# Kernel tuning notes

Measured on AMD Instinct MI355X. Metric: run time of the kernel, lower is better.

Reference implementation:

```python
import jax, jax.numpy as jnp
import numpy as np

N0, N1, N2 = 120000, 24000, 6000  # nodes per sampled layer
H1, C1 = 8, 64   # layer1: heads, nhid (concat -> 512)
H2, C2 = 8, 256  # layer2: out heads, code_embed_dim (mean over heads)
D = 256
NEG_SLOPE = 0.2


def gat_conv(x_src, x_dst, src, dst, W, att_src, att_dst, bias, n_tgt, concat):
    H, C = att_src.shape
    h_src = (x_src @ W).reshape(-1, H, C)   # [N_src, H, C]
    h_dst = (x_dst @ W).reshape(-1, H, C)   # [N_tgt, H, C]
    a_src = jnp.einsum('nhc,hc->nh', h_src, att_src)  # [N_src, H]
    a_dst = jnp.einsum('nhc,hc->nh', h_dst, att_dst)  # [N_tgt, H]
    e = a_src[src] + a_dst[dst]                       # [E, H]
    e = jnp.where(e > 0, e, NEG_SLOPE * e)            # LeakyReLU
    # segment softmax over edges grouped by target node
    m = jax.ops.segment_max(e, dst, num_segments=n_tgt)  # [N_tgt, H]
    ex = jnp.exp(e - m[dst])
    denom = jax.ops.segment_sum(ex, dst, num_segments=n_tgt)
    alpha = ex / denom[dst]                           # [E, H]
    msg = alpha[:, :, None] * h_src[src]              # [E, H, C]
    out = jax.ops.segment_sum(msg, dst, num_segments=n_tgt)  # [N_tgt, H, C]
    if concat:
        return out.reshape(n_tgt, H * C) + bias
    return out.mean(axis=1) + bias


def setup_inputs() -> dict:
    key = jax.random.key(0)
    ks = jax.random.split(key, 12)
    E1, E2 = 384000, 96000
    g1 = 1.0 / np.sqrt(D)
    g2 = 1.0 / np.sqrt(H1 * C1)
    return {
        'x': jax.random.normal(ks[0], (N0, D), jnp.float32),
        'src1': jax.random.randint(ks[1], (E1,), 0, N0),
        'dst1': jax.random.randint(ks[2], (E1,), 0, N1),
        'src2': jax.random.randint(ks[3], (E2,), 0, N1),
        'dst2': jax.random.randint(ks[4], (E2,), 0, N2),
        'W1': jax.random.normal(ks[5], (D, H1 * C1), jnp.float32) * g1,
        'att_src1': jax.random.normal(ks[6], (H1, C1), jnp.float32) * 0.1,
        'att_dst1': jax.random.normal(ks[7], (H1, C1), jnp.float32) * 0.1,
        'b1': jnp.zeros((H1 * C1,), jnp.float32),
        'W2': jax.random.normal(ks[8], (H1 * C1, H2 * C2), jnp.float32) * g2,
        'att_src2': jax.random.normal(ks[9], (H2, C2), jnp.float32) * 0.1,
        'att_dst2': jax.random.normal(ks[10], (H2, C2), jnp.float32) * 0.1,
        'b2': jnp.zeros((C2,), jnp.float32),
    }


def reference(x, src1, dst1, src2, dst2, W1, att_src1, att_dst1, b1,
              W2, att_src2, att_dst2, b2):
    # layer 1: bipartite conv (x, x[:N1]), concat heads, then ELU
    x1 = gat_conv(x, x[:N1], src1, dst1, W1, att_src1, att_dst1, b1, N1, True)
    x1 = jax.nn.elu(x1)
    # layer 2: (x1, x1[:N2]), mean over heads
    x2 = gat_conv(x1, x1[:N2], src2, dst2, W2, att_src2, att_dst2, b2, N2, False)
    return x2
```

## Files before the change

### kernel.cpp

```cpp
#include <hip/hip_runtime.h>
#include <hip/hip_bf16.h>
#include <cstdint>

typedef __attribute__((ext_vector_type(8))) short short8;
typedef __attribute__((ext_vector_type(4))) float floatx4;
typedef __hip_bfloat16 bf16;
typedef unsigned short u16;

static constexpr int cN0 = 120000, cN1 = 24000, cN2 = 6000;
static constexpr int cD = 256, cHC1 = 512;
static constexpr int CH1 = 4800;

__device__ __forceinline__ float dot4(float4 a, float4 b) {
  return a.x * b.x + a.y * b.y + a.z * b.z + a.w * b.w;
}

__global__ __launch_bounds__(256)
void gat_prep(const float* __restrict__ W1, const float* __restrict__ W2,
              const float* __restrict__ as1, const float* __restrict__ ad1,
              const float* __restrict__ as2, const float* __restrict__ ad2,
              u16* __restrict__ W1t, u16* __restrict__ W2te,
              float* __restrict__ wts1, float* __restrict__ wtd1,
              float* __restrict__ wts2, float* __restrict__ wtd2) {
  __shared__ u16 tile[32][33];
  int b = (int)blockIdx.x;
  if (b < 512) {
    int t = b * 256 + threadIdx.x;
    int n = t >> 8, k = t & 255;
    bf16 v = bf16(W1[(size_t)k * 512 + n]);
    W1t[t] = *(u16*)&v;
    return;
  }
  b -= 512;
  if (b < 1024) {
    int bx = b & 15, by = (b >> 4) & 7, h = b >> 7;
    int kt = bx * 32, ct = by * 32;
    int tx = threadIdx.x & 31, ty4 = (threadIdx.x >> 5) * 4;
#pragma unroll
    for (int i = 0; i < 4; i++) {
      int k = kt + ty4 + i, c = ct + tx;
      bf16 v = bf16(W2[(size_t)k * 2048 + h * 256 + c]);
      tile[ty4 + i][tx] = *(u16*)&v;
    }
    __syncthreads();
#pragma unroll
    for (int i = 0; i < 4; i++) {
      int c = ct + ty4 + i, k = kt + tx;
      W2te[(size_t)c * 4096 + h * 512 + k] = tile[tx][ty4 + i];
    }
    return;
  }
  b -= 1024;
  int lane = threadIdx.x & 63;
  int K, Ch, ldw, task;
  const float *W, *as, *ad;
  float *ws, *wd;
  if (b < 512) {
    K = 256; Ch = 64; ldw = 512; W = W1; as = as1; ad = ad1; ws = wts1; wd = wtd1;
    task = b * 4 + (threadIdx.x >> 6);
  } else {
    b -= 512;
    K = 512; Ch = 256; ldw = 2048; W = W2; as = as2; ad = ad2; ws = wts2; wd = wtd2;
    task = b * 4 + (threadIdx.x >> 6);
  }
  if (task >= 8 * K) return;
  int h = task / K, k = task - h * K;
  const float* Wr = W + (size_t)k * ldw + h * Ch;
  const float* asp = as + h * Ch;
  const float* adp = ad + h * Ch;
  float ss = 0.f, dd = 0.f;
  for (int c = lane; c < Ch; c += 64) {
    float wv = Wr[c];
    ss += wv * asp[c];
    dd += wv * adp[c];
  }
#pragma unroll
  for (int o = 32; o; o >>= 1) { ss += __shfl_down(ss, o); dd += __shfl_down(dd, o); }
  if (lane == 0) { ws[task] = ss; wd[task] = dd; }
}

#define RSTAGE(HALF, MASK)                                              \
  {                                                                     \
    _Pragma("unroll") for (int j = 0; j < HALF; j++) {                  \
      float send = (lane & MASK) ? v[j] : v[j + HALF];                  \
      float rcv = __shfl_xor(send, MASK);                               \
      v[j] = ((lane & MASK) ? v[j + HALF] : v[j]) + rcv;                \
    }                                                                   \
  }

__global__ __launch_bounds__(256)
void gat_scores_reg(const float* __restrict__ x, const float* __restrict__ wsrc,
                    const float* __restrict__ wdst, float* __restrict__ a_s,
                    float* __restrict__ a_d, int M, int MD) {
  int lane = threadIdx.x & 63;
  int wv = (blockIdx.x * 256 + threadIdx.x) >> 6;
  int nw = (gridDim.x * 256) >> 6;
  float4 w[16];
#pragma unroll
  for (int j = 0; j < 8; j++) {
    w[j]     = *(const float4*)&wsrc[j * 256 + lane * 4];
    w[j + 8] = *(const float4*)&wdst[j * 256 + lane * 4];
  }
  for (int row = wv; row < M; row += nw) {
    float4 xv = *(const float4*)&x[(size_t)row * 256 + lane * 4];
    float v[16];
#pragma unroll
    for (int j = 0; j < 16; j++) v[j] = dot4(xv, w[j]);
    RSTAGE(8, 1) RSTAGE(4, 2) RSTAGE(2, 4) RSTAGE(1, 8)
    v[0] += __shfl_xor(v[0], 16);
    v[0] += __shfl_xor(v[0], 32);
    if (lane < 16) {
      int o = ((lane & 1) << 3) | ((lane & 2) << 1) | ((lane & 4) >> 1) | ((lane & 8) >> 3);
      if (o < 8) a_s[row * 8 + o] = v[0];
      else if (row < MD) a_d[row * 8 + (o - 8)] = v[0];
    }
  }
}

__global__ __launch_bounds__(256)
void gat_scores_w512(const float* __restrict__ x, const float* __restrict__ wsrc,
                     const float* __restrict__ wdst, float* __restrict__ a_s,
                     float* __restrict__ a_d, int M, int MD) {
  __shared__ float wl[16 * 512];
  int tid = threadIdx.x;
#pragma unroll
  for (int base = 0; base < 8192; base += 1024) {
    int idx = base + tid * 4;
    int j = idx >> 9, c = idx & 511;
    *(float4*)&wl[idx] = (j < 8) ? *(const float4*)&wsrc[j * 512 + c]
                                 : *(const float4*)&wdst[(j - 8) * 512 + c];
  }
  __syncthreads();
  int lane = tid & 63;
  int wv = (blockIdx.x * 256 + tid) >> 6;
  int nw = (gridDim.x * 256) >> 6;
  for (int row = wv; row < M; row += nw) {
    float4 xa = *(const float4*)&x[(size_t)row * 512 + lane * 4];
    float4 xb = *(const float4*)&x[(size_t)row * 512 + 256 + lane * 4];
    float v[16];
#pragma unroll
    for (int j = 0; j < 16; j++) {
      float4 wa = *(const float4*)&wl[j * 512 + lane * 4];
      float4 wb = *(const float4*)&wl[j * 512 + 256 + lane * 4];
      v[j] = dot4(xa, wa) + dot4(xb, wb);
    }
    RSTAGE(8, 1) RSTAGE(4, 2) RSTAGE(2, 4) RSTAGE(1, 8)
    v[0] += __shfl_xor(v[0], 16);
    v[0] += __shfl_xor(v[0], 32);
    if (lane < 16) {
      int o = ((lane & 1) << 3) | ((lane & 2) << 1) | ((lane & 4) >> 1) | ((lane & 8) >> 3);
      if (o < 8) a_s[row * 8 + o] = v[0];
      else if (row < MD) a_d[row * 8 + (o - 8)] = v[0];
    }
  }
}

__global__ __launch_bounds__(256)
void gat_hist(const int* __restrict__ dstv, int* __restrict__ cnt, int E) {
  int t = blockIdx.x * 256 + threadIdx.x;
  if (t < E) atomicAdd(&cnt[dstv[t]], 1);
}

__global__ __launch_bounds__(1024)
void gat_scan1(const int* __restrict__ cnt, int* __restrict__ off,
               int* __restrict__ bsum, int n) {
  __shared__ int wsum[16];
  int t = threadIdx.x, lane = t & 63, wid = t >> 6;
  int idx = blockIdx.x * 1024 + t;
  int v = (idx < n) ? cnt[idx] : 0;
  int x = v;
#pragma unroll
  for (int d = 1; d < 64; d <<= 1) { int y = __shfl_up(x, d); if (lane >= d) x += y; }
  if (lane == 63) wsum[wid] = x;
  __syncthreads();
  if (t < 16) {
    int s = wsum[t];
#pragma unroll
    for (int d = 1; d < 16; d <<= 1) { int y = __shfl_up(s, d); if (t >= d) s += y; }
    wsum[t] = s;
  }
  __syncthreads();
  int excl = (wid ? wsum[wid - 1] : 0) + x - v;
  if (idx < n) off[idx] = excl;
  if (t == 1023) bsum[blockIdx.x] = wsum[15];
}

__global__ __launch_bounds__(256)
void gat_scan3(int* __restrict__ off, const int* __restrict__ bsum, int n, int nb) {
  int i = blockIdx.x * 256 + threadIdx.x;
  int blk = (blockIdx.x * 256) >> 10;
  int add = 0;
  for (int b = 0; b < blk; b++) add += bsum[b];
  if (i < n) off[i] += add;
  if (i == 0) {
    int tot = 0;
    for (int b = 0; b < nb; b++) tot += bsum[b];
    off[n] = tot;
  }
}

__global__ __launch_bounds__(256)
void gat_scatter_edge(const int* __restrict__ src, const int* __restrict__ dstv,
                      const float* __restrict__ a_s, const float* __restrict__ a_d,
                      const int* __restrict__ off, int* __restrict__ cur,
                      int* __restrict__ srcs, float* __restrict__ exs, int E) {
  int t = blockIdx.x * 256 + threadIdx.x;
  if (t >= E) return;
  int s = src[t], d = dstv[t];
  int slot = off[d] + atomicAdd(&cur[d], 1);
  srcs[slot] = s;
  const float* as = a_s + (size_t)s * 8;
  const float* ad = a_d + (size_t)d * 8;
  float4 s0 = *(const float4*)as, s1 = *(const float4*)(as + 4);
  float4 d0 = *(const float4*)ad, d1 = *(const float4*)(ad + 4);
  float ev[8] = { s0.x + d0.x, s0.y + d0.y, s0.z + d0.z, s0.w + d0.w,
                  s1.x + d1.x, s1.y + d1.y, s1.z + d1.z, s1.w + d1.w };
  float exv[8];
#pragma unroll
  for (int h = 0; h < 8; h++) {
    float e = ev[h];
    e = e > 0.f ? e : 0.2f * e;
    exv[h] = expf(e);
  }
  float4* op = (float4*)(exs + (size_t)slot * 8);
  op[0] = make_float4(exv[0], exv[1], exv[2], exv[3]);
  op[1] = make_float4(exv[4], exv[5], exv[6], exv[7]);
}

__global__ __launch_bounds__(256)
void gat_denom(const float* __restrict__ exs, const int* __restrict__ off,
               float* __restrict__ den, int N) {
  int lane = threadIdx.x & 63;
  int d = blockIdx.x * 4 + (threadIdx.x >> 6);
  if (d >= N) return;
  int beg = off[d], end = off[d + 1];
  float s = 0.f;
  for (size_t idx = (size_t)beg * 8 + lane; idx < (size_t)end * 8; idx += 64)
    s += exs[idx];
#pragma unroll
  for (int o = 32; o >= 8; o >>= 1) s += __shfl_down(s, o);
  if (lane < 8) den[(size_t)d * 8 + lane] = s;
}

template<int CDIM>
__global__ __launch_bounds__(CDIM)
void gat_gather(const float* __restrict__ x, const float* __restrict__ exs,
                const float* __restrict__ den, const int* __restrict__ off,
                const int* __restrict__ srcs, u16* __restrict__ agg, int d0) {
  int d = d0 + blockIdx.x, t = threadIdx.x;
  int beg = off[d], end = off[d + 1];
  float inv[8];
#pragma unroll
  for (int j = 0; j < 8; j++) {
    float dv = den[(size_t)d * 8 + j];
    inv[j] = dv > 0.f ? 1.f / dv : 0.f;
  }
  float acc[8] = {};
  const float* xb = x + t;
  int i = beg;
  for (; i + 4 <= end; i += 4) {
    int s0 = srcs[i], s1 = srcs[i + 1], s2 = srcs[i + 2], s3 = srcs[i + 3];
    float xv0 = xb[(size_t)s0 * CDIM];
    float xv1 = xb[(size_t)s1 * CDIM];
    float xv2 = xb[(size_t)s2 * CDIM];
    float xv3 = xb[(size_t)s3 * CDIM];
    float4 e0a = *(const float4*)&exs[(size_t)i * 8];
    float4 e0b = *(const float4*)&exs[(size_t)i * 8 + 4];
    float4 e1a = *(const float4*)&exs[(size_t)(i + 1) * 8];
    float4 e1b = *(const float4*)&exs[(size_t)(i + 1) * 8 + 4];
    float4 e2a = *(const float4*)&exs[(size_t)(i + 2) * 8];
    float4 e2b = *(const float4*)&exs[(size_t)(i + 2) * 8 + 4];
    float4 e3a = *(const float4*)&exs[(size_t)(i + 3) * 8];
    float4 e3b = *(const float4*)&exs[(size_t)(i + 3) * 8 + 4];
    acc[0] += e0a.x * xv0 + e1a.x * xv1 + e2a.x * xv2 + e3a.x * xv3;
    acc[1] += e0a.y * xv0 + e1a.y * xv1 + e2a.y * xv2 + e3a.y * xv3;
    acc[2] += e0a.z * xv0 + e1a.z * xv1 + e2a.z * xv2 + e3a.z * xv3;
    acc[3] += e0a.w * xv0 + e1a.w * xv1 + e2a.w * xv2 + e3a.w * xv3;
    acc[4] += e0b.x * xv0 + e1b.x * xv1 + e2b.x * xv2 + e3b.x * xv3;
    acc[5] += e0b.y * xv0 + e1b.y * xv1 + e2b.y * xv2 + e3b.y * xv3;
    acc[6] += e0b.z * xv0 + e1b.z * xv1 + e2b.z * xv2 + e3b.z * xv3;
    acc[7] += e0b.w * xv0 + e1b.w * xv1 + e2b.w * xv2 + e3b.w * xv3;
  }
  for (; i < end; i++) {
    int s = srcs[i];
    float xv = xb[(size_t)s * CDIM];
    float4 ea = *(const float4*)&exs[(size_t)i * 8];
    float4 eb = *(const float4*)&exs[(size_t)i * 8 + 4];
    acc[0] += ea.x * xv; acc[1] += ea.y * xv; acc[2] += ea.z * xv; acc[3] += ea.w * xv;
    acc[4] += eb.x * xv; acc[5] += eb.y * xv; acc[6] += eb.z * xv; acc[7] += eb.w * xv;
  }
  u16* ap = agg + (size_t)blockIdx.x * (8 * CDIM) + t;
#pragma unroll
  for (int j = 0; j < 8; j++) {
    bf16 v = bf16(acc[j] * inv[j]);
    ap[(size_t)j * CDIM] = *(u16*)&v;
  }
}

template<int BN, int EPI>
__global__ __launch_bounds__(256)
void gat_gemm(const u16* __restrict__ A, long lda, const u16* __restrict__ Bt, long ldb,
              float* __restrict__ C, long ldc, int M, int K,
              const float* __restrict__ bias, int zA, int zB, long zC, int zBias) {
  __shared__ __align__(16) u16 Al[64 * 64];
  __shared__ __align__(16) u16 Bl[BN * 64];
  const int tid = threadIdx.x;
  const int bm = blockIdx.x << 6;
  const int n0 = blockIdx.y * BN;
  const int z = blockIdx.z;
  const u16* Ab = A + (size_t)z * zA;
  const u16* Bb = Bt + (size_t)z * zB + (size_t)n0 * ldb;
  const int wid = tid >> 6, lane = tid & 63;
  const int wm = (wid & 1) << 5, wn = (wid >> 1) * (BN / 2);
  const int q = lane >> 4, r = lane & 15;
  constexpr int NJ = BN / 32;
  floatx4 acc[2][NJ] = {};
  const int arow = tid >> 3;
  const int chunk = tid & 7;
  const int acol = chunk << 3;
  for (int k0 = 0; k0 < K; k0 += 64) {
    __syncthreads();
#pragma unroll
    for (int rr = 0; rr < 2; rr++) {
      int row = arow + rr * 32;
      int gr = bm + row; if (gr >= M) gr = M - 1;
      *(uint4*)&Al[row * 64 + ((chunk ^ (row & 7)) << 3)] =
          *(const uint4*)&Ab[(size_t)gr * lda + k0 + acol];
    }
#pragma unroll
    for (int rr = 0; rr < BN / 32; rr++) {
      int row = arow + rr * 32;
      *(uint4*)&Bl[row * 64 + ((chunk ^ (row & 7)) << 3)] =
          *(const uint4*)&Bb[(size_t)row * ldb + k0 + acol];
    }
    __syncthreads();
#pragma unroll
    for (int kk = 0; kk < 64; kk += 32) {
      const int cs = (((kk >> 3) + q) ^ (r & 7)) << 3;
      short8 af[2], bfr[NJ];
#pragma unroll
      for (int i = 0; i < 2; i++)  af[i]  = *(const short8*)&Al[(wm + i * 16 + r) * 64 + cs];
#pragma unroll
      for (int j = 0; j < NJ; j++) bfr[j] = *(const short8*)&Bl[(wn + j * 16 + r) * 64 + cs];
#pragma unroll
      for (int i = 0; i < 2; i++)
#pragma unroll
        for (int j = 0; j < NJ; j++)
          acc[i][j] = __builtin_amdgcn_mfma_f32_16x16x32_bf16(af[i], bfr[j], acc[i][j], 0, 0, 0);
    }
  }
#pragma unroll
  for (int i = 0; i < 2; i++)
#pragma unroll
    for (int j = 0; j < NJ; j++) {
      int gn = n0 + wn + j * 16 + r;
      float bv = (EPI == 1) ? bias[zBias * z + gn] : 0.f;
#pragma unroll
      for (int t2 = 0; t2 < 4; t2++) {
        int gm = bm + wm + i * 16 + q * 4 + t2;
        if (gm < M) {
          float v = acc[i][j][t2];
          if (EPI == 1) { v += bv; v = v > 0.f ? v : expm1f(v); }
          C[(size_t)z * zC + (size_t)gm * ldc + gn] = v;
        }
      }
    }
}

__global__ __launch_bounds__(256)
void gat_reduce4(const float* __restrict__ p, const float* __restrict__ bias,
                 float* __restrict__ out, int MN) {
  int t = blockIdx.x * 256 + threadIdx.x;
  if (t >= MN) return;
  size_t mn = (size_t)MN;
  float v = p[t] + p[t + mn] + p[t + 2 * mn] + p[t + 3 * mn];
  out[t] = v * 0.125f + bias[t & 255];
}

extern "C" void kernel_launch(void* const* d_in, const int* in_sizes, int n_in,
                              void* d_out, int out_size, void* d_ws, size_t ws_size,
                              hipStream_t stream) {
  const float* x    = (const float*)d_in[0];
  const int* src1   = (const int*)d_in[1];
  const int* dst1   = (const int*)d_in[2];
  const int* src2   = (const int*)d_in[3];
  const int* dst2   = (const int*)d_in[4];
  const float* W1   = (const float*)d_in[5];
  const float* atts1 = (const float*)d_in[6];
  const float* attd1 = (const float*)d_in[7];
  const float* b1   = (const float*)d_in[8];
  const float* W2   = (const float*)d_in[9];
  const float* atts2 = (const float*)d_in[10];
  const float* attd2 = (const float*)d_in[11];
  const float* b2   = (const float*)d_in[12];
  const int E1 = in_sizes[1], E2 = in_sizes[3];

  uint8_t* p = (uint8_t*)d_ws;
  auto alloc = [&](size_t b) { uint8_t* r = p; p += (b + 255) & ~(size_t)255; return r; };
  auto al = [](size_t b) { return (b + 255) & ~(size_t)255; };
  float* x1   = (float*)alloc((size_t)cN1 * cHC1 * 4);
  u16*   W1t  = (u16*)alloc((size_t)512 * 256 * 2);
  u16*   W2te = (u16*)alloc((size_t)256 * 4096 * 2);
  float* wts1 = (float*)alloc(8 * 256 * 4);
  float* wtd1 = (float*)alloc(8 * 256 * 4);
  float* wts2 = (float*)alloc(8 * 512 * 4);
  float* wtd2 = (float*)alloc(8 * 512 * 4);
  uint8_t* scratch = p;
  size_t usedPersist = (size_t)(scratch - (uint8_t*)d_ws);

  auto phaseA = [&](size_t m1) {
    return al(m1 * 2048 * 2) + al((size_t)cN0 * 32) + al((size_t)cN1 * 32) +
           al((size_t)E1 * 32) + al((size_t)E1 * 4) + al((size_t)(cN1 + 1) * 4) +
           al(256) + al((size_t)cN1 * 32) + 2 * al((size_t)cN1 * 4);
  };
  int M1 = (usedPersist + phaseA(cN1) <= ws_size) ? cN1 : CH1;
  int nch1 = cN1 / M1;
  u16*   aggA  = (u16*)alloc((size_t)M1 * 2048 * 2);
  float* a_s1  = (float*)alloc((size_t)cN0 * 32);
  float* a_d1  = (float*)alloc((size_t)cN1 * 32);
  float* exs1  = (float*)alloc((size_t)E1 * 32);
  int*   srcs1 = (int*)alloc((size_t)E1 * 4);
  int*   off1  = (int*)alloc((size_t)(cN1 + 1) * 4);
  int*   bsum1 = (int*)alloc(256);
  float* den1  = (float*)alloc((size_t)cN1 * 32);
  uint8_t* zA = p;
  int*   cnt1 = (int*)alloc((size_t)cN1 * 4);
  int*   cur1 = (int*)alloc((size_t)cN1 * 4);
  size_t zAbytes = (size_t)(p - zA);

  auto phaseB = [&](size_t m2) {
    return al(m2 * 4096 * 2) + al(4ull * m2 * 256 * 4) + al((size_t)cN1 * 32) +
           al((size_t)cN2 * 32) + al((size_t)E2 * 32) + al((size_t)E2 * 4) +
           al((size_t)(cN2 + 1) * 4) + al(256) + al((size_t)cN2 * 32) +
           2 * al((size_t)cN2 * 4);
  };
  int M2 = (usedPersist + phaseB(6000) <= ws_size) ? 6000 : 3000;
  int nch2 = 6000 / M2;
  p = scratch;
  u16*   aggB  = (u16*)alloc((size_t)M2 * 4096 * 2);
  float* pbuf  = (float*)alloc(4ull * M2 * 256 * 4);
  float* a_s2  = (float*)alloc((size_t)cN1 * 32);
  float* a_d2  = (float*)alloc((size_t)cN2 * 32);
  float* exs2  = (float*)alloc((size_t)E2 * 32);
  int*   srcs2 = (int*)alloc((size_t)E2 * 4);
  int*   off2  = (int*)alloc((size_t)(cN2 + 1) * 4);
  int*   bsum2 = (int*)alloc(256);
  float* den2  = (float*)alloc((size_t)cN2 * 32);
  uint8_t* zB = p;
  int*   cnt2 = (int*)alloc((size_t)cN2 * 4);
  int*   cur2 = (int*)alloc((size_t)cN2 * 4);
  size_t zBbytes = (size_t)(p - zB);

  gat_prep<<<3072, 256, 0, stream>>>(W1, W2, atts1, attd1, atts2, attd2,
                                     W1t, W2te, wts1, wtd1, wts2, wtd2);

  hipMemsetAsync(zA, 0, zAbytes, stream);
  gat_scores_reg<<<1024, 256, 0, stream>>>(x, wts1, wtd1, a_s1, a_d1, cN0, cN1);
  gat_hist<<<(E1 + 255) / 256, 256, 0, stream>>>(dst1, cnt1, E1);
  {
    int nb = (cN1 + 1023) / 1024;
    gat_scan1<<<nb, 1024, 0, stream>>>(cnt1, off1, bsum1, cN1);
    gat_scan3<<<(cN1 + 255) / 256, 256, 0, stream>>>(off1, bsum1, cN1, nb);
  }
  gat_scatter_edge<<<(E1 + 255) / 256, 256, 0, stream>>>(src1, dst1, a_s1, a_d1, off1, cur1, srcs1, exs1, E1);
  gat_denom<<<(cN1 + 3) / 4, 256, 0, stream>>>(exs1, off1, den1, cN1);
  for (int c = 0; c < nch1; c++) {
    int d0 = c * M1;
    gat_gather<256><<<M1, 256, 0, stream>>>(x, exs1, den1, off1, srcs1, aggA, d0);
    gat_gemm<64, 1><<<dim3(M1 / 64, 1, 8), 256, 0, stream>>>(
        aggA, 2048, W1t, 256, x1 + (size_t)d0 * cHC1, cHC1,
        M1, 256, b1, 256, 64 * 256, 64, 64);
  }

  hipMemsetAsync(zB, 0, zBbytes, stream);
  gat_scores_w512<<<512, 256, 0, stream>>>(x1, wts2, wtd2, a_s2, a_d2, cN1, cN2);
  gat_hist<<<(E2 + 255) / 256, 256, 0, stream>>>(dst2, cnt2, E2);
  {
    int nb = (cN2 + 1023) / 1024;
    gat_scan1<<<nb, 1024, 0, stream>>>(cnt2, off2, bsum2, cN2);
    gat_scan3<<<(cN2 + 255) / 256, 256, 0, stream>>>(off2, bsum2, cN2, nb);
  }
  gat_scatter_edge<<<(E2 + 255) / 256, 256, 0, stream>>>(src2, dst2, a_s2, a_d2, off2, cur2, srcs2, exs2, E2);
  gat_denom<<<(cN2 + 3) / 4, 256, 0, stream>>>(exs2, off2, den2, cN2);
  for (int c = 0; c < nch2; c++) {
    int d0 = c * M2;
    gat_gather<512><<<M2, 512, 0, stream>>>(x1, exs2, den2, off2, srcs2, aggB, d0);
    gat_gemm<128, 0><<<dim3((M2 + 63) / 64, 2, 4), 256, 0, stream>>>(
        aggB, 4096, W2te, 4096, pbuf, 256,
        M2, 1024, nullptr, 1024, 1024, (long)M2 * 256, 0);
    gat_reduce4<<<(M2 * 256 + 255) / 256, 256, 0, stream>>>(
        pbuf, b2, (float*)d_out + (size_t)d0 * 256, M2 * 256);
  }
}
```

Before: 483.9 us.

## Fuse softmax denominator into edge scatter and drop layer-2 split-K reduce

The softmax denominator is now accumulated with per-head atomicAdd inside the edge scatter kernel, which removes the separate per-node reduction kernel. The zeroed region now includes the denominator buffers. The layer-2 GEMM no longer splits K=4096 four ways into a partial buffer followed by a reduce kernel. It runs the full K in one pass, with a new epilogue that scales by 1/8, adds the bias and writes straight to the output. This removes a launch and the partial-buffer traffic, but it trades away K-parallelism (fewer blocks) and adds atomic contention on hot destination nodes.

```diff
diff --git a/kernel.cpp b/kernel.cpp
--- a/kernel.cpp
+++ b/kernel.cpp
@@ -6,6 +6,7 @@
 typedef __attribute__((ext_vector_type(4))) float floatx4;
 typedef __hip_bfloat16 bf16;
 typedef unsigned short u16;
+typedef unsigned int u32;
 
 static constexpr int cN0 = 120000, cN1 = 24000, cN2 = 6000;
 static constexpr int cD = 256, cHC1 = 512;
@@ -203,7 +204,8 @@
 void gat_scatter_edge(const int* __restrict__ src, const int* __restrict__ dstv,
                       const float* __restrict__ a_s, const float* __restrict__ a_d,
                       const int* __restrict__ off, int* __restrict__ cur,
-                      int* __restrict__ srcs, float* __restrict__ exs, int E) {
+                      int* __restrict__ srcs, float* __restrict__ exs,
+                      float* __restrict__ den, int E) {
   int t = blockIdx.x * 256 + threadIdx.x;
   if (t >= E) return;
   int s = src[t], d = dstv[t];
@@ -216,30 +218,17 @@
   float ev[8] = { s0.x + d0.x, s0.y + d0.y, s0.z + d0.z, s0.w + d0.w,
                   s1.x + d1.x, s1.y + d1.y, s1.z + d1.z, s1.w + d1.w };
   float exv[8];
+  float* dp = den + (size_t)d * 8;
 #pragma unroll
   for (int h = 0; h < 8; h++) {
     float e = ev[h];
     e = e > 0.f ? e : 0.2f * e;
     exv[h] = expf(e);
+    atomicAdd(&dp[h], exv[h]);
   }
   float4* op = (float4*)(exs + (size_t)slot * 8);
   op[0] = make_float4(exv[0], exv[1], exv[2], exv[3]);
   op[1] = make_float4(exv[4], exv[5], exv[6], exv[7]);
-}
-
-__global__ __launch_bounds__(256)
-void gat_denom(const float* __restrict__ exs, const int* __restrict__ off,
-               float* __restrict__ den, int N) {
-  int lane = threadIdx.x & 63;
-  int d = blockIdx.x * 4 + (threadIdx.x >> 6);
-  if (d >= N) return;
-  int beg = off[d], end = off[d + 1];
-  float s = 0.f;
-  for (size_t idx = (size_t)beg * 8 + lane; idx < (size_t)end * 8; idx += 64)
-    s += exs[idx];
-#pragma unroll
-  for (int o = 32; o >= 8; o >>= 1) s += __shfl_down(s, o);
-  if (lane < 8) den[(size_t)d * 8 + lane] = s;
 }
 
 template<int CDIM>
@@ -354,27 +343,18 @@
 #pragma unroll
     for (int j = 0; j < NJ; j++) {
       int gn = n0 + wn + j * 16 + r;
-      float bv = (EPI == 1) ? bias[zBias * z + gn] : 0.f;
+      float bv = (EPI >= 1) ? bias[zBias * z + gn] : 0.f;
 #pragma unroll
       for (int t2 = 0; t2 < 4; t2++) {
         int gm = bm + wm + i * 16 + q * 4 + t2;
         if (gm < M) {
           float v = acc[i][j][t2];
           if (EPI == 1) { v += bv; v = v > 0.f ? v : expm1f(v); }
+          if (EPI == 2) { v = v * 0.125f + bv; }
           C[(size_t)z * zC + (size_t)gm * ldc + gn] = v;
         }
       }
     }
-}
-
-__global__ __launch_bounds__(256)
-void gat_reduce4(const float* __restrict__ p, const float* __restrict__ bias,
-                 float* __restrict__ out, int MN) {
-  int t = blockIdx.x * 256 + threadIdx.x;
-  if (t >= MN) return;
-  size_t mn = (size_t)MN;
-  float v = p[t] + p[t + mn] + p[t + 2 * mn] + p[t + 3 * mn];
-  out[t] = v * 0.125f + bias[t & 255];
 }
 
 extern "C" void kernel_launch(void* const* d_in, const int* in_sizes, int n_in,
@@ -422,14 +402,14 @@
   int*   srcs1 = (int*)alloc((size_t)E1 * 4);
   int*   off1  = (int*)alloc((size_t)(cN1 + 1) * 4);
   int*   bsum1 = (int*)alloc(256);
-  float* den1  = (float*)alloc((size_t)cN1 * 32);
   uint8_t* zA = p;
   int*   cnt1 = (int*)alloc((size_t)cN1 * 4);
   int*   cur1 = (int*)alloc((size_t)cN1 * 4);
+  float* den1 = (float*)alloc((size_t)cN1 * 32);
   size_t zAbytes = (size_t)(p - zA);
 
   auto phaseB = [&](size_t m2) {
-    return al(m2 * 4096 * 2) + al(4ull * m2 * 256 * 4) + al((size_t)cN1 * 32) +
+    return al(m2 * 4096 * 2) + al((size_t)cN1 * 32) +
            al((size_t)cN2 * 32) + al((size_t)E2 * 32) + al((size_t)E2 * 4) +
            al((size_t)(cN2 + 1) * 4) + al(256) + al((size_t)cN2 * 32) +
            2 * al((size_t)cN2 * 4);
@@ -438,17 +418,16 @@
   int nch2 = 6000 / M2;
   p = scratch;
   u16*   aggB  = (u16*)alloc((size_t)M2 * 4096 * 2);
-  float* pbuf  = (float*)alloc(4ull * M2 * 256 * 4);
   float* a_s2  = (float*)alloc((size_t)cN1 * 32);
   float* a_d2  = (float*)alloc((size_t)cN2 * 32);
   float* exs2  = (float*)alloc((size_t)E2 * 32);
   int*   srcs2 = (int*)alloc((size_t)E2 * 4);
   int*   off2  = (int*)alloc((size_t)(cN2 + 1) * 4);
   int*   bsum2 = (int*)alloc(256);
-  float* den2  = (float*)alloc((size_t)cN2 * 32);
   uint8_t* zB = p;
   int*   cnt2 = (int*)alloc((size_t)cN2 * 4);
   int*   cur2 = (int*)alloc((size_t)cN2 * 4);
+  float* den2 = (float*)alloc((size_t)cN2 * 32);
   size_t zBbytes = (size_t)(p - zB);
 
   gat_prep<<<3072, 256, 0, stream>>>(W1, W2, atts1, attd1, atts2, attd2,
@@ -462,8 +441,8 @@
     gat_scan1<<<nb, 1024, 0, stream>>>(cnt1, off1, bsum1, cN1);
     gat_scan3<<<(cN1 + 255) / 256, 256, 0, stream>>>(off1, bsum1, cN1, nb);
   }
-  gat_scatter_edge<<<(E1 + 255) / 256, 256, 0, stream>>>(src1, dst1, a_s1, a_d1, off1, cur1, srcs1, exs1, E1);
-  gat_denom<<<(cN1 + 3) / 4, 256, 0, stream>>>(exs1, off1, den1, cN1);
+  gat_scatter_edge<<<(E1 + 255) / 256, 256, 0, stream>>>(
+      src1, dst1, a_s1, a_d1, off1, cur1, srcs1, exs1, den1, E1);
   for (int c = 0; c < nch1; c++) {
     int d0 = c * M1;
     gat_gather<256><<<M1, 256, 0, stream>>>(x, exs1, den1, off1, srcs1, aggA, d0);
@@ -480,15 +459,13 @@
     gat_scan1<<<nb, 1024, 0, stream>>>(cnt2, off2, bsum2, cN2);
     gat_scan3<<<(cN2 + 255) / 256, 256, 0, stream>>>(off2, bsum2, cN2, nb);
   }
-  gat_scatter_edge<<<(E2 + 255) / 256, 256, 0, stream>>>(src2, dst2, a_s2, a_d2, off2, cur2, srcs2, exs2, E2);
-  gat_denom<<<(cN2 + 3) / 4, 256, 0, stream>>>(exs2, off2, den2, cN2);
+  gat_scatter_edge<<<(E2 + 255) / 256, 256, 0, stream>>>(
+      src2, dst2, a_s2, a_d2, off2, cur2, srcs2, exs2, den2, E2);
   for (int c = 0; c < nch2; c++) {
     int d0 = c * M2;
     gat_gather<512><<<M2, 512, 0, stream>>>(x1, exs2, den2, off2, srcs2, aggB, d0);
-    gat_gemm<128, 0><<<dim3((M2 + 63) / 64, 2, 4), 256, 0, stream>>>(
-        aggB, 4096, W2te, 4096, pbuf, 256,
-        M2, 1024, nullptr, 1024, 1024, (long)M2 * 256, 0);
-    gat_reduce4<<<(M2 * 256 + 255) / 256, 256, 0, stream>>>(
-        pbuf, b2, (float*)d_out + (size_t)d0 * 256, M2 * 256);
-  }
-}
+    gat_gemm<64, 2><<<dim3((M2 + 63) / 64, 4, 1), 256, 0, stream>>>(
+        aggB, 4096, W2te, 4096, (float*)d_out + (size_t)d0 * 256, 256,
+        M2, 4096, b2, 0, 0, 0, 0);
+  }
+}
```

New measurement: 698.1 us. +44.3%, slower.
